# Kernel tuning notes

Hardware: AMD Instinct MI355X
Metric: run time of the kernel (lower is better)

Reference implementation:

```python
import jax, jax.numpy as jnp
import numpy as np

C = 16  # number of classes (matches batch_ids fill_max)
XMIN, XMAX = 1e-37, 1.0 - 1e-5

def setup_inputs() -> dict:
    key = jax.random.key(0)
    k1, k2 = jax.random.split(key)
    hidden = jax.random.normal(k1, (65536, 512), dtype=jnp.float32)
    batch_ids = jax.random.randint(k2, (65536,), 0, C, dtype=jnp.int64)
    return {"hidden": hidden, "batch_ids": batch_ids, "d": 64}

def reference(hidden, batch_ids, d):
    N, D = hidden.shape
    seg = lambda v: jax.ops.segment_sum(v, batch_ids, num_segments=C)
    counts = seg(jnp.ones((N,), hidden.dtype))                  # [C]
    means = seg(hidden) / counts[:, None]                       # [C, D]
    # within-class sum of squared deviations, per feature dim
    withins = seg((hidden - means[batch_ids]) ** 2)             # [C, D]
    # pairwise: global mean of pair is (m_i+m_j)/2, so each class's between
    # term is ((m_i-m_j)/2)^2; weighted by counts it sums to that * (n_i+n_j)
    half_diff = (means[:, None, :] - means[None, :, :]) * 0.5   # [C, C, D]
    pair_counts = counts[:, None] + counts[None, :]             # [C, C]
    pair_between = half_diff * half_diff * pair_counts[:, :, None]
    pair_within = withins[:, None, :] + withins[None, :, :]
    d2 = pair_counts - 2.0
    d2 = jnp.where(d2 == 0.0, 1e-5, d2)
    x = pair_between / (pair_between + pair_within)
    x = jnp.clip(x, XMIN, XMAX)
    a = jnp.full_like(x, 0.5)                                   # d1/2
    b = jnp.broadcast_to((d2 * 0.5)[:, :, None], x.shape)       # d2/2
    xbetainc = jax.scipy.special.betainc(a, b, x)               # [C, C, D]
    top_k, _ = jax.lax.top_k(xbetainc, d)                       # [C, C, d]
    per_pair = jnp.sum(jnp.log(top_k), axis=-1)                 # [C, C]
    mask = jnp.triu(jnp.ones((C, C), dtype=bool), k=1)          # pairs i<j
    total = jnp.sum(jnp.where(mask, per_pair, jnp.zeros_like(per_pair)))
    return -total
```

## Files before the change

kernel.cpp:

```cpp
#include <hip/hip_runtime.h>
#include <math.h>

#define NUM_C 16
#define DIMS 512
#define CHUNKS 32

__device__ inline void atomAddF(float* p, float v) { unsafeAtomicAdd(p, v); }

__global__ __launch_bounds__(256) void k_counts(const int* __restrict__ bids,
                                                int* __restrict__ counts, int n) {
    __shared__ int h[NUM_C];
    const int tid = threadIdx.x;
    if (tid < NUM_C) h[tid] = 0;
    __syncthreads();
    const int i0 = (blockIdx.x * 256 + tid) * 4;
    if (i0 + 3 < n) {
        int4 c4 = *reinterpret_cast<const int4*>(bids + i0);
        atomicAdd(&h[c4.x], 1); atomicAdd(&h[c4.y], 1);
        atomicAdd(&h[c4.z], 1); atomicAdd(&h[c4.w], 1);
    }
    __syncthreads();
    if (tid < NUM_C) atomicAdd(&counts[tid], h[tid]);
}

__global__ void k_prefix(const int* __restrict__ counts,
                         int* __restrict__ offs, int* __restrict__ gcur) {
    if (threadIdx.x == 0) {
        int acc = 0;
        for (int c = 0; c < NUM_C; ++c) { offs[c] = acc; gcur[c] = acc; acc += counts[c]; }
    }
}

__global__ __launch_bounds__(256) void k_scatter(const int* __restrict__ bids,
                                                 int* __restrict__ gcur,
                                                 int* __restrict__ perm, int n) {
    __shared__ int lh[NUM_C], lb[NUM_C], lc[NUM_C];
    const int tid = threadIdx.x;
    if (tid < NUM_C) lh[tid] = 0;
    __syncthreads();
    const int i0 = (blockIdx.x * 256 + tid) * 4;
    int4 c4 = make_int4(0, 0, 0, 0);
    const bool ok = (i0 + 3 < n);
    if (ok) {
        c4 = *reinterpret_cast<const int4*>(bids + i0);
        atomicAdd(&lh[c4.x], 1); atomicAdd(&lh[c4.y], 1);
        atomicAdd(&lh[c4.z], 1); atomicAdd(&lh[c4.w], 1);
    }
    __syncthreads();
    if (tid < NUM_C) { lb[tid] = atomicAdd(&gcur[tid], lh[tid]); lc[tid] = 0; }
    __syncthreads();
    if (ok) {
        perm[lb[c4.x] + atomicAdd(&lc[c4.x], 1)] = i0;
        perm[lb[c4.y] + atomicAdd(&lc[c4.y], 1)] = i0 + 1;
        perm[lb[c4.z] + atomicAdd(&lc[c4.z], 1)] = i0 + 2;
        perm[lb[c4.w] + atomicAdd(&lc[c4.w], 1)] = i0 + 3;
    }
}

__global__ __launch_bounds__(256) void k_segsum(const float* __restrict__ hidden,
                                                const int* __restrict__ perm,
                                                const int* __restrict__ counts,
                                                const int* __restrict__ offs,
                                                float* __restrict__ gsum,
                                                float* __restrict__ gsq) {
    const int tid = threadIdx.x;
    const int c = blockIdx.x & (NUM_C - 1);
    const int chunk = blockIdx.x >> 4;
    const int cnt = counts[c];
    const int base = offs[c];
    const int len = (cnt + CHUNKS - 1) / CHUNKS;
    const int lo = chunk * len;
    const int hi = min(lo + len, cnt);
    const int half = tid >> 7, ht = tid & 127;

    float4 s = {0.f, 0.f, 0.f, 0.f}, q = {0.f, 0.f, 0.f, 0.f};
#define LOADROW(r) (*(reinterpret_cast<const float4*>(hidden + (size_t)(r) * DIMS) + ht))
#define ACC(v) { s.x += (v).x; s.y += (v).y; s.z += (v).z; s.w += (v).w; \
                 q.x += (v).x*(v).x; q.y += (v).y*(v).y; q.z += (v).z*(v).z; q.w += (v).w*(v).w; }
    int k = lo + half;
    for (; k + 6 < hi; k += 8) {
        const int r0 = perm[base + k],     r1 = perm[base + k + 2];
        const int r2 = perm[base + k + 4], r3 = perm[base + k + 6];
        const float4 v0 = LOADROW(r0), v1 = LOADROW(r1);
        const float4 v2 = LOADROW(r2), v3 = LOADROW(r3);
        ACC(v0); ACC(v1); ACC(v2); ACC(v3);
    }
    for (; k < hi; k += 2) {
        const int r0 = perm[base + k];
        const float4 v0 = LOADROW(r0);
        ACC(v0);
    }
#undef LOADROW
#undef ACC

    __shared__ float red[128 * 8];
    if (half == 1) {
        float* p = &red[ht * 8];
        p[0] = s.x; p[1] = s.y; p[2] = s.z; p[3] = s.w;
        p[4] = q.x; p[5] = q.y; p[6] = q.z; p[7] = q.w;
    }
    __syncthreads();
    if (half == 0) {
        const float* p = &red[ht * 8];
        s.x += p[0]; s.y += p[1]; s.z += p[2]; s.w += p[3];
        q.x += p[4]; q.y += p[5]; q.z += p[6]; q.w += p[7];
        float* gs = gsum + c * DIMS + 4 * ht;
        float* gq = gsq  + c * DIMS + 4 * ht;
        atomAddF(gs + 0, s.x); atomAddF(gs + 1, s.y);
        atomAddF(gs + 2, s.z); atomAddF(gs + 3, s.w);
        atomAddF(gq + 0, q.x); atomAddF(gq + 1, q.y);
        atomAddF(gq + 2, q.z); atomAddF(gq + 3, q.w);
    }
}

__global__ __launch_bounds__(256) void k_final(const float* __restrict__ gsum,
                                               const float* __restrict__ gsq,
                                               const int* __restrict__ counts,
                                               float* __restrict__ means,
                                               float* __restrict__ withins) {
    const int idx = blockIdx.x * 256 + threadIdx.x;
    if (idx >= NUM_C * DIMS) return;
    const int c = idx >> 9;
    const float n = (float)counts[c];
    const float s = gsum[idx];
    const float m = s / n;
    means[idx] = m;
    const float w = gsq[idx] - s * m;
    withins[idx] = w > 0.f ? w : 0.f;
}

__global__ __launch_bounds__(512) void k_pairs(const float* __restrict__ means,
                                               const float* __restrict__ withins,
                                               const int* __restrict__ counts,
                                               const int* __restrict__ dptr,
                                               float* __restrict__ out) {
    __shared__ float xs[DIMS];
    __shared__ float wsum[8];
    const int tid = threadIdx.x;

    int p = blockIdx.x, i = 0, rem = p;
    while (rem >= NUM_C - 1 - i) { rem -= NUM_C - 1 - i; ++i; }
    const int j = i + 1 + rem;

    const float pc = (float)(counts[i] + counts[j]);

    {
        const float mi = means[i * DIMS + tid], mj = means[j * DIMS + tid];
        const float hd = (mi - mj) * 0.5f;
        const float between = hd * hd * pc;
        const float within = withins[i * DIMS + tid] + withins[j * DIMS + tid];
        float x = between / (between + within);
        if (!(x >= 1e-37f)) x = 1e-37f;
        const float XM = 1.0f - 1e-5f;
        if (x > XM) x = XM;
        xs[tid] = x;
    }

    for (int kk = 2; kk <= DIMS; kk <<= 1) {
        for (int jj = kk >> 1; jj > 0; jj >>= 1) {
            __syncthreads();
            const int ixj = tid ^ jj;
            if (ixj > tid) {
                const float va = xs[tid], vb = xs[ixj];
                const bool sw = ((tid & kk) == 0) ? (va < vb) : (va > vb);
                if (sw) { xs[tid] = vb; xs[ixj] = va; }
            }
        }
    }
    __syncthreads();

    const int d = *dptr;
    float d2 = pc - 2.0f;
    if (d2 == 0.0f) d2 = 1e-5f;
    const float b = d2 * 0.5f;
    const float bm1 = b - 1.0f;
    const float invb = 1.0f / b;
    const float ln2overB = 0.69314718f
        - (0.5f * (1.14472989f - logf(b)) + log1pf(invb * (0.125f + 0.0078125f * invb)));

    const int sub = tid & 7;
    const int rounds = (d + 63) >> 6;
    float part = 0.f;
    for (int r = 0; r < rounds; ++r) {
        const int q = (tid >> 3) + (r << 6);
        const bool act = (q < d);
        const float x = xs[act ? q : 0];
        const float rt = sqrtf(x);
        const float h = rt * (1.0f / 256.0f);
        float acc = 0.f;
        for (int k = sub; k <= 256; k += 8) {
            const float sv = (float)k * h;
            const float w = (k == 0 || k == 256) ? 1.f : ((k & 1) ? 4.f : 2.f);
            acc += w * __expf(bm1 * log1pf(-sv * sv));
        }
        acc += __shfl_down(acc, 4, 64);
        acc += __shfl_down(acc, 2, 64);
        acc += __shfl_down(acc, 1, 64);
        if (sub == 0 && act) {
            float li = logf(acc * h * (1.0f / 3.0f)) + ln2overB;
            part += (li < 0.f) ? li : 0.f;
        }
    }
    for (int off = 32; off > 0; off >>= 1) part += __shfl_down(part, off, 64);
    if ((tid & 63) == 0) wsum[tid >> 6] = part;
    __syncthreads();
    if (tid == 0) {
        float t = 0.f;
        for (int w = 0; w < 8; ++w) t += wsum[w];
        atomAddF(out, -t);
    }
}

extern "C" void kernel_launch(void* const* d_in, const int* in_sizes, int n_in,
                              void* d_out, int out_size, void* d_ws, size_t ws_size,
                              hipStream_t stream) {
    const float* hidden = (const float*)d_in[0];
    const int* bids = (const int*)d_in[1];
    const int* dptr = (const int*)d_in[2];
    float* out = (float*)d_out;
    const int N = in_sizes[1];

    char* ws = (char*)d_ws;
    int* counts   = (int*)(ws + 0);
    int* offs     = (int*)(ws + 256);
    int* gcur     = (int*)(ws + 512);
    float* gsum   = (float*)(ws + 1024);
    float* gsq    = (float*)(ws + 33792);
    float* means  = (float*)(ws + 66560);
    float* withins= (float*)(ws + 99328);
    int* perm     = (int*)(ws + 132096);

    hipMemsetAsync(d_ws, 0, 66560, stream);
    hipMemsetAsync(d_out, 0, sizeof(float), stream);

    const int nb = (N + 1023) / 1024;
    k_counts <<<nb, 256, 0, stream>>>(bids, counts, N);
    k_prefix <<<1, 64, 0, stream>>>(counts, offs, gcur);
    k_scatter<<<nb, 256, 0, stream>>>(bids, gcur, perm, N);
    k_segsum <<<NUM_C * CHUNKS, 256, 0, stream>>>(hidden, perm, counts, offs, gsum, gsq);
    k_final  <<<(NUM_C * DIMS + 255) / 256, 256, 0, stream>>>(gsum, gsq, counts, means, withins);
    k_pairs  <<<NUM_C * (NUM_C - 1) / 2, 512, 0, stream>>>(means, withins, counts, dptr, out);
}
```

Baseline: 237.9 us.

## Drop count/prefix passes with per-class bucket regions and fuse finalize into pairs

Replaces the count, prefix and scatter kernels with a single scatter pass. That pass writes each class into its own N-sized region of the permutation buffer, so the running atomic counters end up holding the class counts. The finalize kernel is folded into the pairs kernel, which computes means and within-class sums directly from the sums and squared sums. Output zeroing moves into the scatter kernel, and segsum doubles its chunk count for more parallelism. Together this cuts launches and memsets from eight to four, at the cost of a 16x larger permutation workspace and a little redundant per-pair arithmetic.

```diff
diff --git a/kernel.cpp b/kernel.cpp
--- a/kernel.cpp
+++ b/kernel.cpp
@@ -3,39 +3,18 @@
 
 #define NUM_C 16
 #define DIMS 512
-#define CHUNKS 32
+#define CHUNKS 64
 
 __device__ inline void atomAddF(float* p, float v) { unsafeAtomicAdd(p, v); }
 
-__global__ __launch_bounds__(256) void k_counts(const int* __restrict__ bids,
-                                                int* __restrict__ counts, int n) {
-    __shared__ int h[NUM_C];
-    const int tid = threadIdx.x;
-    if (tid < NUM_C) h[tid] = 0;
-    __syncthreads();
-    const int i0 = (blockIdx.x * 256 + tid) * 4;
-    if (i0 + 3 < n) {
-        int4 c4 = *reinterpret_cast<const int4*>(bids + i0);
-        atomicAdd(&h[c4.x], 1); atomicAdd(&h[c4.y], 1);
-        atomicAdd(&h[c4.z], 1); atomicAdd(&h[c4.w], 1);
-    }
-    __syncthreads();
-    if (tid < NUM_C) atomicAdd(&counts[tid], h[tid]);
-}
-
-__global__ void k_prefix(const int* __restrict__ counts,
-                         int* __restrict__ offs, int* __restrict__ gcur) {
-    if (threadIdx.x == 0) {
-        int acc = 0;
-        for (int c = 0; c < NUM_C; ++c) { offs[c] = acc; gcur[c] = acc; acc += counts[c]; }
-    }
-}
-
-__global__ __launch_bounds__(256) void k_scatter(const int* __restrict__ bids,
-                                                 int* __restrict__ gcur,
-                                                 int* __restrict__ perm, int n) {
+
+__global__ __launch_bounds__(256) void k_scatter1p(const int* __restrict__ bids,
+                                                   int* __restrict__ gcur,
+                                                   int* __restrict__ perm,
+                                                   float* __restrict__ out, int n) {
     __shared__ int lh[NUM_C], lb[NUM_C], lc[NUM_C];
     const int tid = threadIdx.x;
+    if (blockIdx.x == 0 && tid == 0) out[0] = 0.f;
     if (tid < NUM_C) lh[tid] = 0;
     __syncthreads();
     const int i0 = (blockIdx.x * 256 + tid) * 4;
@@ -47,7 +26,10 @@
         atomicAdd(&lh[c4.z], 1); atomicAdd(&lh[c4.w], 1);
     }
     __syncthreads();
-    if (tid < NUM_C) { lb[tid] = atomicAdd(&gcur[tid], lh[tid]); lc[tid] = 0; }
+    if (tid < NUM_C) {
+        lb[tid] = tid * n + atomicAdd(&gcur[tid], lh[tid]);
+        lc[tid] = 0;
+    }
     __syncthreads();
     if (ok) {
         perm[lb[c4.x] + atomicAdd(&lc[c4.x], 1)] = i0;
@@ -59,15 +41,14 @@
 
 __global__ __launch_bounds__(256) void k_segsum(const float* __restrict__ hidden,
                                                 const int* __restrict__ perm,
-                                                const int* __restrict__ counts,
-                                                const int* __restrict__ offs,
+                                                const int* __restrict__ gcur,
                                                 float* __restrict__ gsum,
-                                                float* __restrict__ gsq) {
+                                                float* __restrict__ gsq, int n) {
     const int tid = threadIdx.x;
     const int c = blockIdx.x & (NUM_C - 1);
     const int chunk = blockIdx.x >> 4;
-    const int cnt = counts[c];
-    const int base = offs[c];
+    const int cnt = gcur[c];
+    const int base = c * n;
     const int len = (cnt + CHUNKS - 1) / CHUNKS;
     const int lo = chunk * len;
     const int hi = min(lo + len, cnt);
@@ -113,25 +94,9 @@
     }
 }
 
-__global__ __launch_bounds__(256) void k_final(const float* __restrict__ gsum,
+__global__ __launch_bounds__(512) void k_pairs(const float* __restrict__ gsum,
                                                const float* __restrict__ gsq,
-                                               const int* __restrict__ counts,
-                                               float* __restrict__ means,
-                                               float* __restrict__ withins) {
-    const int idx = blockIdx.x * 256 + threadIdx.x;
-    if (idx >= NUM_C * DIMS) return;
-    const int c = idx >> 9;
-    const float n = (float)counts[c];
-    const float s = gsum[idx];
-    const float m = s / n;
-    means[idx] = m;
-    const float w = gsq[idx] - s * m;
-    withins[idx] = w > 0.f ? w : 0.f;
-}
-
-__global__ __launch_bounds__(512) void k_pairs(const float* __restrict__ means,
-                                               const float* __restrict__ withins,
-                                               const int* __restrict__ counts,
+                                               const int* __restrict__ gcur,
                                                const int* __restrict__ dptr,
                                                float* __restrict__ out) {
     __shared__ float xs[DIMS];
@@ -142,13 +107,18 @@
     while (rem >= NUM_C - 1 - i) { rem -= NUM_C - 1 - i; ++i; }
     const int j = i + 1 + rem;
 
-    const float pc = (float)(counts[i] + counts[j]);
+    const float ni = (float)gcur[i], nj = (float)gcur[j];
+    const float pc = ni + nj;
 
     {
-        const float mi = means[i * DIMS + tid], mj = means[j * DIMS + tid];
+        const float si = gsum[i * DIMS + tid];
+        const float sj = gsum[j * DIMS + tid];
+        const float mi = si / ni, mj = sj / nj;
+        float wi = gsq[i * DIMS + tid] - si * mi;  wi = wi > 0.f ? wi : 0.f;
+        float wj = gsq[j * DIMS + tid] - sj * mj;  wj = wj > 0.f ? wj : 0.f;
         const float hd = (mi - mj) * 0.5f;
         const float between = hd * hd * pc;
-        const float within = withins[i * DIMS + tid] + withins[j * DIMS + tid];
+        const float within = wi + wj;
         float x = between / (between + within);
         if (!(x >= 1e-37f)) x = 1e-37f;
         const float XM = 1.0f - 1e-5f;
@@ -221,23 +191,15 @@
     const int N = in_sizes[1];
 
     char* ws = (char*)d_ws;
-    int* counts   = (int*)(ws + 0);
-    int* offs     = (int*)(ws + 256);
-    int* gcur     = (int*)(ws + 512);
-    float* gsum   = (float*)(ws + 1024);
-    float* gsq    = (float*)(ws + 33792);
-    float* means  = (float*)(ws + 66560);
-    float* withins= (float*)(ws + 99328);
-    int* perm     = (int*)(ws + 132096);
-
-    hipMemsetAsync(d_ws, 0, 66560, stream);
-    hipMemsetAsync(d_out, 0, sizeof(float), stream);
+    int*   gcur = (int*)(ws + 0);
+    float* gsum = (float*)(ws + 256);
+    float* gsq  = (float*)(ws + 33024);
+    int*   perm = (int*)(ws + 65792);
+
+    hipMemsetAsync(d_ws, 0, 65792, stream);
 
     const int nb = (N + 1023) / 1024;
-    k_counts <<<nb, 256, 0, stream>>>(bids, counts, N);
-    k_prefix <<<1, 64, 0, stream>>>(counts, offs, gcur);
-    k_scatter<<<nb, 256, 0, stream>>>(bids, gcur, perm, N);
-    k_segsum <<<NUM_C * CHUNKS, 256, 0, stream>>>(hidden, perm, counts, offs, gsum, gsq);
-    k_final  <<<(NUM_C * DIMS + 255) / 256, 256, 0, stream>>>(gsum, gsq, counts, means, withins);
-    k_pairs  <<<NUM_C * (NUM_C - 1) / 2, 512, 0, stream>>>(means, withins, counts, dptr, out);
-}
+    k_scatter1p<<<nb, 256, 0, stream>>>(bids, gcur, perm, out, N);
+    k_segsum  <<<NUM_C * CHUNKS, 256, 0, stream>>>(hidden, perm, gcur, gsum, gsq, N);
+    k_pairs   <<<NUM_C * (NUM_C - 1) / 2, 512, 0, stream>>>(gsum, gsq, gcur, dptr, out);
+}
```

Result: no change. 240.1 us (+0.9%).
